# Kernel optimization log

Hardware: AMD Instinct MI355X
Metric: run time of the kernel (lower is better)

## Reference

```python
import jax, jax.numpy as jnp
import numpy as np

K = 16  # neighbors, from self.k in the module


def _pconv(x, w, b):
    # 1x1 Conv1d: x (B,C,N), w (O,C), b (O,)
    return jnp.einsum('oc,bcn->bon', w, x) + b[None, :, None]


def _gather_neighbors(xn, idx):
    # xn (B,N,C), idx (B,N,K) int -> (B,N,K,C)
    return jax.vmap(lambda xb, ib: xb[ib])(xn, idx)


def _local_maxpool(x, idx):
    # x (B,C,N) -> (B,N,C): max over K gathered neighbor features
    xn = jnp.transpose(x, (0, 2, 1))
    return jnp.max(_gather_neighbors(xn, idx), axis=2)


def setup_inputs() -> dict:
    key = jax.random.key(0)
    ks = jax.random.split(key, 20)
    B, N = 8, 2048
    def w(k, shape, fan_in):
        return jax.random.normal(k, shape, dtype=jnp.float32) / np.sqrt(fan_in)
    inp = {
        'pts': jax.random.normal(ks[0], (B, N, 3), dtype=jnp.float32),
        'w1a': w(ks[1], (64, 12), 12), 'b1a': jnp.zeros((64,), jnp.float32),
        'w1b': w(ks[2], (64, 64), 64), 'b1b': jnp.zeros((64,), jnp.float32),
        'w1c': w(ks[3], (64, 64), 64), 'b1c': jnp.zeros((64,), jnp.float32),
        'lin1_w': w(ks[4], (64, 64), 64), 'lin1_b': jnp.zeros((64,), jnp.float32),
        'conv1_w': w(ks[5], (128, 64), 64), 'conv1_b': jnp.zeros((128,), jnp.float32),
        'lin2_w': w(ks[6], (128, 128), 128), 'lin2_b': jnp.zeros((128,), jnp.float32),
        'conv2_w': w(ks[7], (1024, 128), 128), 'conv2_b': jnp.zeros((1024,), jnp.float32),
        'w2a': w(ks[8], (512, 1024), 1024), 'b2a': jnp.zeros((512,), jnp.float32),
        'w2b': w(ks[9], (512, 512), 512), 'b2b': jnp.zeros((512,), jnp.float32),
    }
    return inp


def reference(pts, w1a, b1a, w1b, b1b, w1c, b1c, lin1_w, lin1_b,
              conv1_w, conv1_b, lin2_w, lin2_b, conv2_w, conv2_b,
              w2a, b2a, w2b, b2b):
    B, N, _ = pts.shape
    pts_t = jnp.transpose(pts, (0, 2, 1))  # (B,3,N)
    # kNN: topk of negative squared pairwise distance (self is first neighbor)
    sq = jnp.sum(pts_t * pts_t, axis=1)                      # (B,N)
    inner = jnp.einsum('bdn,bdm->bnm', pts_t, pts_t)         # (B,N,N)
    neg_dist = 2.0 * inner - sq[:, :, None] - sq[:, None, :]
    idx = jax.lax.top_k(neg_dist, K)[1]                      # (B,N,K) int32
    # local_cov: outer product of first two gathered neighbor coords
    neigh = _gather_neighbors(pts, idx)                      # (B,N,K,3)
    cov = jnp.einsum('bni,bnj->bnij', neigh[:, :, 0], neigh[:, :, 1])
    cov = cov.reshape(B, N, 9)
    x = jnp.concatenate([pts_t, jnp.transpose(cov, (0, 2, 1))], axis=1)  # (B,12,N)
    # mlp1
    x = jax.nn.relu(_pconv(x, w1a, b1a))
    x = jax.nn.relu(_pconv(x, w1b, b1b))
    x = jax.nn.relu(_pconv(x, w1c, b1c))
    # graph layer
    x = _local_maxpool(x, idx)                               # (B,N,64)
    x = x @ lin1_w.T + lin1_b                                # (B,N,64)
    x = jnp.transpose(x, (0, 2, 1))                          # (B,64,N)
    x = jax.nn.relu(_pconv(x, conv1_w, conv1_b))             # (B,128,N)
    x = _local_maxpool(x, idx)                               # (B,N,128)
    x = x @ lin2_w.T + lin2_b
    x = jnp.transpose(x, (0, 2, 1))                          # (B,128,N)
    x = _pconv(x, conv2_w, conv2_b)                          # (B,1024,N)
    # global max pool
    x = jnp.max(x, axis=2, keepdims=True)                    # (B,1024,1)
    # mlp2
    x = jax.nn.relu(_pconv(x, w2a, b2a))
    x = _pconv(x, w2b, b2b)                                  # (B,512,1)
    return jnp.transpose(x, (0, 2, 1))                       # (B,1,512)
```

## Files before the change

kernel.cpp:

```cpp
#include <hip/hip_runtime.h>

#define BB 8
#define NN 2048
#define KK 16
#define QT 32
#define NSLICE 16
#define SLEN 128
#define KP 18

typedef short bf16x8 __attribute__((ext_vector_type(8)));
typedef float f32x4 __attribute__((ext_vector_type(4)));
typedef unsigned short ushort8v __attribute__((ext_vector_type(8)));

__device__ __forceinline__ float4 f4max(float4 a, float4 b) {
  return make_float4(fmaxf(a.x, b.x), fmaxf(a.y, b.y), fmaxf(a.z, b.z), fmaxf(a.w, b.w));
}

__device__ __forceinline__ unsigned short f2bf(float x) {
  union { float f; unsigned u; } v; v.f = x;
  unsigned r = v.u + 0x7fffu + ((v.u >> 16) & 1u);
  return (unsigned short)(r >> 16);
}
__device__ __forceinline__ float bf2f(unsigned short h) {
  union { unsigned u; float f; } v; v.u = ((unsigned)h) << 16;
  return v.f;
}

__global__ __launch_bounds__(512) void knn_kernel(const float* __restrict__ pts,
                                                  int* __restrict__ knn_idx) {
  __shared__ float4 sp[NN];
  __shared__ unsigned char  pk[NSLICE][QT][KP];
  __shared__ unsigned short s1i[4][QT][16];
  const int b = blockIdx.x & 7;
  const int tile = blockIdx.x >> 3;
  const int tid = threadIdx.x;
  const int q = tid & 31;
  const int s = tid >> 5;

  for (int i = tid; i < NN; i += 512) {
    float x = pts[(size_t)(b * NN + i) * 3 + 0];
    float y = pts[(size_t)(b * NN + i) * 3 + 1];
    float z = pts[(size_t)(b * NN + i) * 3 + 2];
    sp[i] = make_float4(x, y, z, x * x + y * y + z * z);
  }
  __syncthreads();

  {
    const float4 pq = sp[tile * QT + q];
    const float qx = 2.f * pq.x, qy = 2.f * pq.y, qz = 2.f * pq.z;
    unsigned qk[KP];
#pragma unroll
    for (int j = 0; j < KP; ++j) qk[j] = 0u;
    const int m0 = s * SLEN;
    for (int mb = 0; mb < SLEN; mb += 8) {
      float4 c[8];
#pragma unroll
      for (int u = 0; u < 8; ++u) c[u] = sp[m0 + mb + u];
#pragma unroll
      for (int u = 0; u < 8; ++u) {
        const float v = fmaf(qx, c[u].x, fmaf(qy, c[u].y, fmaf(qz, c[u].z, -c[u].w)));
        unsigned uu = __float_as_uint(v);
        unsigned key = uu ^ ((unsigned)(((int)uu) >> 31) | 0x80000000u);
        unsigned run = (key & 0xFFFFFF00u) | (unsigned)(255 - (mb + u));
#pragma unroll
        for (int j = 0; j < KP; ++j) {
          const unsigned hi = max(qk[j], run);
          const unsigned lo = min(qk[j], run);
          qk[j] = hi; run = lo;
        }
      }
    }
#pragma unroll
    for (int j = 0; j < KP; ++j) pk[s][q][j] = (unsigned char)(qk[j] & 0xFFu);
  }
  __syncthreads();

  if (tid < 128) {
    const int q2 = tid & 31, pr = tid >> 5;
    const float4 pm = sp[tile * QT + q2];
    const float qx = 2.f * pm.x, qy = 2.f * pm.y, qz = 2.f * pm.z;
    float mv[16]; int mi[16];
#pragma unroll
    for (int j = 0; j < 16; ++j) { mv[j] = -3.0e38f; mi[j] = 0; }
#pragma unroll 1
    for (int ss = 4 * pr; ss < 4 * pr + 4; ++ss) {
      const int base = ss * SLEN;
#pragma unroll 1
      for (int j = 0; j < KP; ++j) {
        const int id = base + 255 - (int)pk[ss][q2][j];
        const float4 c = sp[id];
        const float v = fmaf(qx, c.x, fmaf(qy, c.y, fmaf(qz, c.z, -c.w)));
        if (v > mv[15]) {
          mv[15] = v; mi[15] = id;
#pragma unroll
          for (int t = 15; t > 0; --t) {
            if (mv[t] > mv[t - 1]) {
              float tv = mv[t]; mv[t] = mv[t - 1]; mv[t - 1] = tv;
              int ti = mi[t]; mi[t] = mi[t - 1]; mi[t - 1] = ti;
            }
          }
        }
      }
    }
#pragma unroll
    for (int j = 0; j < 16; ++j) s1i[pr][q2][j] = (unsigned short)mi[j];
  }
  __syncthreads();

  if (tid < QT) {
    const float4 pm = sp[tile * QT + tid];
    const float qx = 2.f * pm.x, qy = 2.f * pm.y, qz = 2.f * pm.z;
    float mv[16]; int mi[16];
#pragma unroll
    for (int j = 0; j < 16; ++j) { mv[j] = -3.0e38f; mi[j] = 0; }
#pragma unroll 1
    for (int pr = 0; pr < 4; ++pr) {
#pragma unroll 1
      for (int j = 0; j < 16; ++j) {
        const int id = s1i[pr][tid][j];
        const float4 c = sp[id];
        const float v = fmaf(qx, c.x, fmaf(qy, c.y, fmaf(qz, c.z, -c.w)));
        if (v <= mv[15]) break;
        mv[15] = v; mi[15] = id;
#pragma unroll
        for (int t = 15; t > 0; --t) {
          if (mv[t] > mv[t - 1]) {
            float tv = mv[t]; mv[t] = mv[t - 1]; mv[t - 1] = tv;
            int ti = mi[t]; mi[t] = mi[t - 1]; mi[t - 1] = ti;
          }
        }
      }
    }
    const int nq = tile * QT + tid;
#pragma unroll
    for (int j = 0; j < 16; ++j) knn_idx[(size_t)(b * NN + nq) * KK + j] = mi[j];
  }
}

__global__ __launch_bounds__(128) void wcomp_kernel(
    const float* __restrict__ lin1_w, const float* __restrict__ lin1_b,
    const float* __restrict__ conv1_w, const float* __restrict__ conv1_b,
    const float* __restrict__ lin2_w, const float* __restrict__ lin2_b,
    const float* __restrict__ conv2_w, const float* __restrict__ conv2_b,
    unsigned short* __restrict__ w1hi, unsigned short* __restrict__ w1lo,
    float* __restrict__ b1p,
    unsigned short* __restrict__ w2hi, unsigned short* __restrict__ w2lo,
    float* __restrict__ b2p) {
  if (blockIdx.x < 128) {
    const int o = blockIdx.x;
    const int c = threadIdx.x;
    if (c < 64) {
      float acc = 0.f;
#pragma unroll 8
      for (int k = 0; k < 64; ++k) acc += conv1_w[o * 64 + k] * lin1_w[k * 64 + c];
      const unsigned short h = f2bf(acc);
      w1hi[o * 64 + c] = h;
      w1lo[o * 64 + c] = f2bf(acc - bf2f(h));
      if (c == 0) {
        float bb = conv1_b[o];
        for (int k = 0; k < 64; ++k) bb += conv1_w[o * 64 + k] * lin1_b[k];
        b1p[o] = bb;
      }
    }
  } else {
    const int o = blockIdx.x - 128;
    const int c = threadIdx.x;
    float acc = 0.f;
#pragma unroll 8
    for (int k = 0; k < 128; ++k) acc += conv2_w[o * 128 + k] * lin2_w[k * 128 + c];
    const unsigned short h = f2bf(acc);
    w2hi[o * 128 + c] = h;
    w2lo[o * 128 + c] = f2bf(acc - bf2f(h));
    if (c == 0) {
      float bb = conv2_b[o];
      for (int k = 0; k < 128; ++k) bb += conv2_w[o * 128 + k] * lin2_b[k];
      b2p[o] = bb;
    }
  }
}

__global__ __launch_bounds__(512, 2) void mlp1_kernel(
    const float* __restrict__ pts, const int* __restrict__ knn_idx,
    const float* __restrict__ w1a, const float* __restrict__ b1a,
    const float* __restrict__ w1b, const float* __restrict__ b1b,
    const float* __restrict__ w1c, const float* __restrict__ b1c,
    float* __restrict__ f1) {
  __shared__ float h1[64][64];
  __shared__ float h2[64][64];
  const int tid = threadIdx.x;
  const int p = tid & 63;
  const int ch = tid >> 6;
  const int b = blockIdx.x & 7;
  const int nc = blockIdx.x >> 3;
  const int bn = b * NN + nc * 64 + p;

  const int n0 = knn_idx[(size_t)bn * KK + 0];
  const int n1 = knn_idx[(size_t)bn * KK + 1];
  const float* pp = &pts[(size_t)bn * 3];
  const float* p0 = &pts[((size_t)(b << 11) + n0) * 3];
  const float* p1 = &pts[((size_t)(b << 11) + n1) * 3];
  float in[12];
  in[0] = pp[0]; in[1] = pp[1]; in[2] = pp[2];
  {
    float a0 = p0[0], a1 = p0[1], a2 = p0[2];
    float c0 = p1[0], c1 = p1[1], c2 = p1[2];
    in[3] = a0 * c0; in[4]  = a0 * c1; in[5]  = a0 * c2;
    in[6] = a1 * c0; in[7]  = a1 * c1; in[8]  = a1 * c2;
    in[9] = a2 * c0; in[10] = a2 * c1; in[11] = a2 * c2;
  }

#pragma unroll
  for (int oi = 0; oi < 8; ++oi) {
    const int o = ch * 8 + oi;
    float a = b1a[o];
#pragma unroll
    for (int c = 0; c < 12; ++c) a += w1a[o * 12 + c] * in[c];
    h1[o][p] = fmaxf(a, 0.f);
  }
  __syncthreads();

  {
    float acc[8];
#pragma unroll
    for (int oi = 0; oi < 8; ++oi) acc[oi] = b1b[ch * 8 + oi];
#pragma unroll 1
    for (int cc = 0; cc < 64; cc += 32) {
      float xr[32];
#pragma unroll
      for (int c = 0; c < 32; ++c) xr[c] = h1[cc + c][p];
#pragma unroll
      for (int oi = 0; oi < 8; ++oi) {
        const int o = ch * 8 + oi;
#pragma unroll
        for (int c = 0; c < 32; ++c) acc[oi] += w1b[o * 64 + cc + c] * xr[c];
      }
    }
    __syncthreads();
#pragma unroll
    for (int oi = 0; oi < 8; ++oi) h2[ch * 8 + oi][p] = fmaxf(acc[oi], 0.f);
  }
  __syncthreads();

  {
    float acc[8];
#pragma unroll
    for (int oi = 0; oi < 8; ++oi) acc[oi] = b1c[ch * 8 + oi];
#pragma unroll 1
    for (int cc = 0; cc < 64; cc += 32) {
      float xr[32];
#pragma unroll
      for (int c = 0; c < 32; ++c) xr[c] = h2[cc + c][p];
#pragma unroll
      for (int oi = 0; oi < 8; ++oi) {
        const int o = ch * 8 + oi;
#pragma unroll
        for (int c = 0; c < 32; ++c) acc[oi] += w1c[o * 64 + cc + c] * xr[c];
      }
    }
#pragma unroll
    for (int oi = 0; oi < 8; ++oi)
      f1[(size_t)bn * 64 + ch * 8 + oi] = fmaxf(acc[oi], 0.f);
  }
}

__global__ __launch_bounds__(256, 2) void gconv1_kernel(
    const float* __restrict__ f1, const int* __restrict__ knn_idx,
    const unsigned short* __restrict__ w1hi, const unsigned short* __restrict__ w1lo,
    const float* __restrict__ b1p, float* __restrict__ f2) {
  __shared__ __align__(16) unsigned short xls[2][64][64];
  const int b = blockIdx.x & 7, nc = blockIdx.x >> 3;
  const int tid = threadIdx.x;
  const int lane = tid & 63, wv = tid >> 6;

  {
    const int p = tid & 63, ch = tid >> 6;
    const int bn = b * NN + nc * 64 + p;
    const int4* idr = (const int4*)&knn_idx[(size_t)bn * KK];
    int4 nb4[4];
#pragma unroll
    for (int q = 0; q < 4; ++q) nb4[q] = idr[q];
    float4 mx[4];
#pragma unroll
    for (int q = 0; q < 4; ++q) mx[q] = make_float4(-3e38f, -3e38f, -3e38f, -3e38f);
#pragma unroll
    for (int j = 0; j < KK; ++j) {
      const int nb = (j & 3) == 0 ? nb4[j >> 2].x : (j & 3) == 1 ? nb4[j >> 2].y
                   : (j & 3) == 2 ? nb4[j >> 2].z : nb4[j >> 2].w;
      const float4* v = (const float4*)&f1[((size_t)(b << 11) + nb) * 64 + ch * 16];
#pragma unroll
      for (int q = 0; q < 4; ++q) mx[q] = f4max(mx[q], v[q]);
    }
    char* basep = (char*)&xls[0][0][0];
#pragma unroll
    for (int s = 0; s < 2; ++s) {
      float xv[8] = {mx[2 * s].x, mx[2 * s].y, mx[2 * s].z, mx[2 * s].w,
                     mx[2 * s + 1].x, mx[2 * s + 1].y, mx[2 * s + 1].z, mx[2 * s + 1].w};
      ushort8v hw, lw;
#pragma unroll
      for (int j = 0; j < 8; ++j) {
        unsigned short h = f2bf(xv[j]);
        hw[j] = h;
        lw[j] = f2bf(xv[j] - bf2f(h));
      }
      const int slot = ch * 2 + s;
      const int swz = slot ^ (p & 7);
      char* dst = basep + p * 128 + swz * 16;
      *(ushort8v*)dst = hw;
      *(ushort8v*)(dst + 8192) = lw;
    }
  }
  __syncthreads();

  const int g = lane >> 4, r = lane & 15;
  const char* basep = (const char*)&xls[0][0][0];
  bf16x8 ah[4][2], al[4][2];
#pragma unroll
  for (int m = 0; m < 4; ++m) {
    const int row = m * 16 + r;
#pragma unroll
    for (int kt = 0; kt < 2; ++kt) {
      const int swz = (kt * 4 + g) ^ (row & 7);
      const char* p = basep + row * 128 + swz * 16;
      ah[m][kt] = *(const bf16x8*)p;
      al[m][kt] = *(const bf16x8*)(p + 8192);
    }
  }
  f32x4 acc[4][2];
#pragma unroll
  for (int m = 0; m < 4; ++m)
#pragma unroll
    for (int nt = 0; nt < 2; ++nt) acc[m][nt] = (f32x4){0.f, 0.f, 0.f, 0.f};

#pragma unroll
  for (int nt = 0; nt < 2; ++nt) {
    const int o = (wv * 2 + nt) * 16 + r;
    const char* wb = (const char*)w1hi + (size_t)o * 128 + g * 16;
    const char* lb = (const char*)w1lo + (size_t)o * 128 + g * 16;
    bf16x8 bh[2], bl[2];
#pragma unroll
    for (int kt = 0; kt < 2; ++kt) {
      bh[kt] = *(const bf16x8*)(wb + kt * 64);
      bl[kt] = *(const bf16x8*)(lb + kt * 64);
    }
#pragma unroll
    for (int kt = 0; kt < 2; ++kt) {
#pragma unroll
      for (int m = 0; m < 4; ++m) {
        acc[m][nt] = __builtin_amdgcn_mfma_f32_16x16x32_bf16(ah[m][kt], bh[kt], acc[m][nt], 0, 0, 0);
        acc[m][nt] = __builtin_amdgcn_mfma_f32_16x16x32_bf16(ah[m][kt], bl[kt], acc[m][nt], 0, 0, 0);
        acc[m][nt] = __builtin_amdgcn_mfma_f32_16x16x32_bf16(al[m][kt], bh[kt], acc[m][nt], 0, 0, 0);
      }
    }
  }
#pragma unroll
  for (int nt = 0; nt < 2; ++nt) {
    const int o = (wv * 2 + nt) * 16 + r;
    const float bias = b1p[o];
#pragma unroll
    for (int m = 0; m < 4; ++m) {
#pragma unroll
      for (int j = 0; j < 4; ++j) {
        const int row = m * 16 + g * 4 + j;
        f2[((size_t)(b * NN + nc * 64 + row)) * 128 + o] = fmaxf(acc[m][nt][j] + bias, 0.f);
      }
    }
  }
}

__global__ __launch_bounds__(256, 2) void gconv2max_kernel(
    const float* __restrict__ f2, const int* __restrict__ knn_idx,
    const unsigned short* __restrict__ w2hi, const unsigned short* __restrict__ w2lo,
    float* __restrict__ pmax) {
  __shared__ __align__(16) unsigned short xls[2][64][128];
  const int b = blockIdx.x & 7, nc = blockIdx.x >> 3;
  const int tid = threadIdx.x;
  const int lane = tid & 63, wv = tid >> 6;

  {
    const int p = tid & 63, ch = tid >> 6;
    const int bn = b * NN + nc * 64 + p;
    const int4* idr = (const int4*)&knn_idx[(size_t)bn * KK];
    int4 nb4[4];
#pragma unroll
    for (int q = 0; q < 4; ++q) nb4[q] = idr[q];
    float4 mx[8];
#pragma unroll
    for (int q = 0; q < 8; ++q) mx[q] = make_float4(-3e38f, -3e38f, -3e38f, -3e38f);
#pragma unroll
    for (int j = 0; j < KK; ++j) {
      const int nb = (j & 3) == 0 ? nb4[j >> 2].x : (j & 3) == 1 ? nb4[j >> 2].y
                   : (j & 3) == 2 ? nb4[j >> 2].z : nb4[j >> 2].w;
      const float4* v = (const float4*)&f2[((size_t)(b << 11) + nb) * 128 + ch * 32];
#pragma unroll
      for (int q = 0; q < 8; ++q) mx[q] = f4max(mx[q], v[q]);
    }
    char* basep = (char*)&xls[0][0][0];
#pragma unroll
    for (int s = 0; s < 4; ++s) {
      float xv[8] = {mx[2 * s].x, mx[2 * s].y, mx[2 * s].z, mx[2 * s].w,
                     mx[2 * s + 1].x, mx[2 * s + 1].y, mx[2 * s + 1].z, mx[2 * s + 1].w};
      ushort8v hw, lw;
#pragma unroll
      for (int j = 0; j < 8; ++j) {
        unsigned short h = f2bf(xv[j]);
        hw[j] = h;
        lw[j] = f2bf(xv[j] - bf2f(h));
      }
      const int slot = ch * 4 + s;
      const int swz = slot ^ (p & 15);
      char* dst = basep + p * 256 + swz * 16;
      *(ushort8v*)dst = hw;
      *(ushort8v*)(dst + 16384) = lw;
    }
  }
  __syncthreads();

  const int g = lane >> 4, r = lane & 15;
  const char* basep = (const char*)&xls[0][0][0];
  float omax[16];
#pragma unroll
  for (int ot = 0; ot < 16; ++ot) omax[ot] = -3e38f;

#pragma unroll
  for (int mg = 0; mg < 2; ++mg) {
    bf16x8 ah[2][4], al[2][4];
#pragma unroll
    for (int m = 0; m < 2; ++m) {
      const int row = (mg * 2 + m) * 16 + r;
#pragma unroll
      for (int kt = 0; kt < 4; ++kt) {
        const int swz = (kt * 4 + g) ^ (row & 15);
        const char* p = basep + row * 256 + swz * 16;
        ah[m][kt] = *(const bf16x8*)p;
        al[m][kt] = *(const bf16x8*)(p + 16384);
      }
    }
#pragma unroll 1
    for (int ot = 0; ot < 16; ++ot) {
      const int o = wv * 256 + ot * 16 + r;
      const char* wb = (const char*)w2hi + (size_t)o * 256 + g * 16;
      const char* lb = (const char*)w2lo + (size_t)o * 256 + g * 16;
      bf16x8 bh[4], bl[4];
#pragma unroll
      for (int kt = 0; kt < 4; ++kt) {
        bh[kt] = *(const bf16x8*)(wb + kt * 64);
        bl[kt] = *(const bf16x8*)(lb + kt * 64);
      }
      f32x4 acc0 = {0.f, 0.f, 0.f, 0.f}, acc1 = {0.f, 0.f, 0.f, 0.f};
#pragma unroll
      for (int kt = 0; kt < 4; ++kt) {
        acc0 = __builtin_amdgcn_mfma_f32_16x16x32_bf16(ah[0][kt], bh[kt], acc0, 0, 0, 0);
        acc1 = __builtin_amdgcn_mfma_f32_16x16x32_bf16(ah[1][kt], bh[kt], acc1, 0, 0, 0);
        acc0 = __builtin_amdgcn_mfma_f32_16x16x32_bf16(ah[0][kt], bl[kt], acc0, 0, 0, 0);
        acc1 = __builtin_amdgcn_mfma_f32_16x16x32_bf16(ah[1][kt], bl[kt], acc1, 0, 0, 0);
        acc0 = __builtin_amdgcn_mfma_f32_16x16x32_bf16(al[0][kt], bh[kt], acc0, 0, 0, 0);
        acc1 = __builtin_amdgcn_mfma_f32_16x16x32_bf16(al[1][kt], bh[kt], acc1, 0, 0, 0);
      }
      float mx = fmaxf(fmaxf(fmaxf(acc0[0], acc0[1]), fmaxf(acc0[2], acc0[3])),
                       fmaxf(fmaxf(acc1[0], acc1[1]), fmaxf(acc1[2], acc1[3])));
      omax[ot] = fmaxf(omax[ot], mx);
    }
  }
#pragma unroll
  for (int ot = 0; ot < 16; ++ot) {
    float v = omax[ot];
    v = fmaxf(v, __shfl_xor(v, 16, 64));
    v = fmaxf(v, __shfl_xor(v, 32, 64));
    omax[ot] = v;
  }
  if (lane < 16) {
#pragma unroll
    for (int ot = 0; ot < 16; ++ot) {
      const int o = wv * 256 + ot * 16 + lane;
      pmax[((size_t)b * 1024 + o) * 32 + nc] = omax[ot];
    }
  }
}

__global__ __launch_bounds__(256) void head_g_kernel(
    const float* __restrict__ pmax, const float* __restrict__ b2p,
    float* __restrict__ gbuf) {
  const int b = blockIdx.x & 7;
  const int o = (blockIdx.x >> 3) * 256 + threadIdx.x;
  const float4* p = (const float4*)&pmax[((size_t)b * 1024 + o) * 32];
  float4 a4 = p[0];
#pragma unroll
  for (int gi = 1; gi < 8; ++gi) a4 = f4max(a4, p[gi]);
  gbuf[b * 1024 + o] = fmaxf(fmaxf(a4.x, a4.y), fmaxf(a4.z, a4.w)) + b2p[o];
}

__global__ __launch_bounds__(256) void head_a_kernel(
    const float* __restrict__ gbuf, const float* __restrict__ w2a,
    const float* __restrict__ b2a, float* __restrict__ hbuf) {
  const int b = blockIdx.x & 7;
  const int k = (blockIdx.x >> 3) * 4 + (threadIdx.x >> 6);
  const int lane = threadIdx.x & 63;
  const float4* wr = (const float4*)&w2a[(size_t)k * 1024];
  const float4* gv = (const float4*)&gbuf[b * 1024];
  float a = 0.f;
#pragma unroll
  for (int i = 0; i < 4; ++i) {
    float4 w = wr[lane + i * 64], xx = gv[lane + i * 64];
    a += w.x * xx.x + w.y * xx.y + w.z * xx.z + w.w * xx.w;
  }
#pragma unroll
  for (int s = 32; s >= 1; s >>= 1) a += __shfl_xor(a, s, 64);
  if (lane == 0) hbuf[b * 512 + k] = fmaxf(a + b2a[k], 0.f);
}

__global__ __launch_bounds__(256) void head_b_kernel(
    const float* __restrict__ hbuf, const float* __restrict__ w2b,
    const float* __restrict__ b2b, float* __restrict__ out) {
  const int b = blockIdx.x & 7;
  const int k = (blockIdx.x >> 3) * 4 + (threadIdx.x >> 6);
  const int lane = threadIdx.x & 63;
  const float4* wr = (const float4*)&w2b[(size_t)k * 512];
  const float4* hv = (const float4*)&hbuf[b * 512];
  float a = 0.f;
#pragma unroll
  for (int i = 0; i < 2; ++i) {
    float4 w = wr[lane + i * 64], xx = hv[lane + i * 64];
    a += w.x * xx.x + w.y * xx.y + w.z * xx.z + w.w * xx.w;
  }
#pragma unroll
  for (int s = 32; s >= 1; s >>= 1) a += __shfl_xor(a, s, 64);
  if (lane == 0) out[b * 512 + k] = a + b2b[k];
}

extern "C" void kernel_launch(void* const* d_in, const int* in_sizes, int n_in,
                              void* d_out, int out_size, void* d_ws, size_t ws_size,
                              hipStream_t stream) {
  const float* pts     = (const float*)d_in[0];
  const float* w1a     = (const float*)d_in[1];
  const float* b1a     = (const float*)d_in[2];
  const float* w1b     = (const float*)d_in[3];
  const float* b1b     = (const float*)d_in[4];
  const float* w1c     = (const float*)d_in[5];
  const float* b1c     = (const float*)d_in[6];
  const float* lin1_w  = (const float*)d_in[7];
  const float* lin1_b  = (const float*)d_in[8];
  const float* conv1_w = (const float*)d_in[9];
  const float* conv1_b = (const float*)d_in[10];
  const float* lin2_w  = (const float*)d_in[11];
  const float* lin2_b  = (const float*)d_in[12];
  const float* conv2_w = (const float*)d_in[13];
  const float* conv2_b = (const float*)d_in[14];
  const float* w2a     = (const float*)d_in[15];
  const float* b2a     = (const float*)d_in[16];
  const float* w2b     = (const float*)d_in[17];
  const float* b2b     = (const float*)d_in[18];

  char* ws = (char*)d_ws;
  int*   knn_idx = (int*)ws;
  float* f1  = (float*)(ws + (1u << 20));
  float* pm  = (float*)(ws + (5u << 20));
  unsigned short* w2hi = (unsigned short*)(ws + (6u << 20));
  unsigned short* w2lo = (unsigned short*)(ws + (6u << 20) + (1u << 18));
  unsigned short* w1hi = (unsigned short*)(ws + (6u << 20) + (2u << 18));
  unsigned short* w1lo = (unsigned short*)(ws + (6u << 20) + (2u << 18) + (1u << 14));
  float* b1p = (float*)(ws + (6u << 20) + (2u << 18) + (2u << 14));
  float* b2p = (float*)(ws + (6u << 20) + (2u << 18) + (3u << 14));
  float* gbuf = (float*)(ws + (7u << 20));
  float* hbuf = (float*)(ws + (7u << 20) + (1u << 16));
  float* f2  = (float*)(ws + (9u << 20));

  wcomp_kernel <<<1152, 128, 0, stream>>>(lin1_w, lin1_b, conv1_w, conv1_b,
                                          lin2_w, lin2_b, conv2_w, conv2_b,
                                          w1hi, w1lo, b1p, w2hi, w2lo, b2p);
  knn_kernel   <<<512, 512, 0, stream>>>(pts, knn_idx);
  mlp1_kernel  <<<256, 512, 0, stream>>>(pts, knn_idx, w1a, b1a, w1b, b1b, w1c, b1c, f1);
  gconv1_kernel<<<256, 256, 0, stream>>>(f1, knn_idx, w1hi, w1lo, b1p, f2);
  gconv2max_kernel<<<256, 256, 0, stream>>>(f2, knn_idx, w2hi, w2lo, pm);
  head_g_kernel<<<32, 256, 0, stream>>>(pm, b2p, gbuf);
  head_a_kernel<<<1024, 256, 0, stream>>>(gbuf, w2a, b2a, hbuf);
  head_b_kernel<<<1024, 256, 0, stream>>>(hbuf, w2b, b2b, (float*)d_out);
}
```

Baseline: 197.8 us.

## Replace per-candidate insertion with sorting network plus bitonic merge in kNN

The kNN selection used to insert each distance key into an 18-entry register list with a compare-exchange chain per candidate. Now each batch of 8 keys is sorted with a 19-comparator network, merged into the running top-16 with an element-wise max against the reversed batch, and cleaned up with a 4-stage bitonic merge. This cuts the number of min/max operations per candidate. The per-slice candidate list also shrinks from 18 to 16 entries, which shortens the refinement pass. That removes the margin that guarded against the truncated 24-bit keys (low byte replaced by an index) ranking near-ties wrongly.

```diff
diff --git a/kernel.cpp b/kernel.cpp
--- a/kernel.cpp
+++ b/kernel.cpp
@@ -6,7 +6,6 @@
 #define QT 32
 #define NSLICE 16
 #define SLEN 128
-#define KP 18
 
 typedef short bf16x8 __attribute__((ext_vector_type(8)));
 typedef float f32x4 __attribute__((ext_vector_type(4)));
@@ -26,10 +25,13 @@
   return v.f;
 }
 
+#define CASD(a, i, j) { unsigned _h = max(a[i], a[j]); unsigned _l = min(a[i], a[j]); \
+                        a[i] = _h; a[j] = _l; }
+
 __global__ __launch_bounds__(512) void knn_kernel(const float* __restrict__ pts,
                                                   int* __restrict__ knn_idx) {
   __shared__ float4 sp[NN];
-  __shared__ unsigned char  pk[NSLICE][QT][KP];
+  __shared__ unsigned char  pk[NSLICE][QT][16];
   __shared__ unsigned short s1i[4][QT][16];
   const int b = blockIdx.x & 7;
   const int tile = blockIdx.x >> 3;
@@ -48,30 +50,40 @@
   {
     const float4 pq = sp[tile * QT + q];
     const float qx = 2.f * pq.x, qy = 2.f * pq.y, qz = 2.f * pq.z;
-    unsigned qk[KP];
-#pragma unroll
-    for (int j = 0; j < KP; ++j) qk[j] = 0u;
+    unsigned A[16];
+#pragma unroll
+    for (int j = 0; j < 16; ++j) A[j] = 0u;
     const int m0 = s * SLEN;
     for (int mb = 0; mb < SLEN; mb += 8) {
       float4 c[8];
 #pragma unroll
       for (int u = 0; u < 8; ++u) c[u] = sp[m0 + mb + u];
+      unsigned kk[8];
 #pragma unroll
       for (int u = 0; u < 8; ++u) {
         const float v = fmaf(qx, c[u].x, fmaf(qy, c[u].y, fmaf(qz, c[u].z, -c[u].w)));
         unsigned uu = __float_as_uint(v);
         unsigned key = uu ^ ((unsigned)(((int)uu) >> 31) | 0x80000000u);
-        unsigned run = (key & 0xFFFFFF00u) | (unsigned)(255 - (mb + u));
-#pragma unroll
-        for (int j = 0; j < KP; ++j) {
-          const unsigned hi = max(qk[j], run);
-          const unsigned lo = min(qk[j], run);
-          qk[j] = hi; run = lo;
+        kk[u] = (key & 0xFFFFFF00u) | (unsigned)(255 - (mb + u));
+      }
+      CASD(kk, 0, 1) CASD(kk, 2, 3) CASD(kk, 4, 5) CASD(kk, 6, 7)
+      CASD(kk, 0, 2) CASD(kk, 1, 3) CASD(kk, 4, 6) CASD(kk, 5, 7)
+      CASD(kk, 1, 2) CASD(kk, 5, 6)
+      CASD(kk, 0, 4) CASD(kk, 1, 5) CASD(kk, 2, 6) CASD(kk, 3, 7)
+      CASD(kk, 2, 4) CASD(kk, 3, 5)
+      CASD(kk, 1, 2) CASD(kk, 3, 4) CASD(kk, 5, 6)
+#pragma unroll
+      for (int i = 8; i < 16; ++i) A[i] = max(A[i], kk[15 - i]);
+#pragma unroll
+      for (int st = 8; st >= 1; st >>= 1) {
+#pragma unroll
+        for (int i = 0; i < 16; ++i) {
+          if ((i & st) == 0) CASD(A, i, i + st)
         }
       }
     }
 #pragma unroll
-    for (int j = 0; j < KP; ++j) pk[s][q][j] = (unsigned char)(qk[j] & 0xFFu);
+    for (int j = 0; j < 16; ++j) pk[s][q][j] = (unsigned char)(A[j] & 0xFFu);
   }
   __syncthreads();
 
@@ -86,7 +98,7 @@
     for (int ss = 4 * pr; ss < 4 * pr + 4; ++ss) {
       const int base = ss * SLEN;
 #pragma unroll 1
-      for (int j = 0; j < KP; ++j) {
+      for (int j = 0; j < 16; ++j) {
         const int id = base + 255 - (int)pk[ss][q2][j];
         const float4 c = sp[id];
         const float v = fmaf(qx, c.x, fmaf(qy, c.y, fmaf(qz, c.z, -c.w)));
```

Result: slower. 215.7 us (+9.1%).
